# Performance work log

Measured on AMD Instinct MI355X. Metric: run time of the kernel, lower is better.

The kernel has to match this reference:

```python
import jax, jax.numpy as jnp
import numpy as np

B, M, N, L = 8, 384, 1536, 20  # batch, checks (detectors), error mechanisms, BP layers
ROW_W = 8  # check-node degree of sparse parity-check matrix H


def setup_inputs() -> dict:
    key = jax.random.key(0)
    ks = jax.random.split(key, 10)
    # Sparse binary check matrix: each row has exactly ROW_W ones (LDPC-like DEM).
    rng = np.random.default_rng(0)
    H_np = np.zeros((M, N), np.float32)
    for i in range(M):
        H_np[i, rng.choice(N, ROW_W, replace=False)] = 1.0
    H = jnp.asarray(H_np)
    llrs = jax.random.uniform(ks[0], (N,), minval=0.5, maxval=2.0)
    syndromes = jax.random.randint(ks[1], (B, M, 1), 0, 2).astype(jnp.float32)
    errors = jax.random.randint(ks[2], (B, N), 0, 2).astype(jnp.float32)
    # Per-layer learned weights (damped so 20 BP iterations stay numerically stable).
    weights_de = jax.random.uniform(ks[3], (L, M, N), minval=0.1, maxval=0.25)
    weights_llr = jax.random.uniform(ks[4], (L, N), minval=0.5, maxval=1.0)
    marg_weights_de = jax.random.uniform(ks[5], (M, N), minval=0.5, maxval=1.0)
    marg_weights_llr = jax.random.uniform(ks[6], (N,), minval=0.5, maxval=1.0)
    residual_weights = jax.random.uniform(ks[7], (L,), minval=0.0, maxval=0.1)
    rhos = jnp.ones((L,), jnp.float32) / L  # init: ones normalized by layers
    return dict(syndromes=syndromes, errors=errors, H=H, llrs=llrs,
                weights_de=weights_de, weights_llr=weights_llr,
                marg_weights_de=marg_weights_de, marg_weights_llr=marg_weights_llr,
                residual_weights=residual_weights, rhos=rhos)


def reference(syndromes, errors, H, llrs, weights_de, weights_llr,
              marg_weights_de, marg_weights_llr, residual_weights, rhos):
    sign = (1.0 - 2.0 * syndromes) * H          # (B,M,N): (-1)^syndrome masked by H
    one_minus_e = 1.0 - errors                  # (B,N)

    def step(msg_dn, per_layer):
        w_de, w_llr, res_w, rho = per_layer
        # --- error (variable) node update ---
        base = H * (llrs * w_llr)                                     # (M,N)
        msg_en = (base + jnp.sum(msg_dn * w_de, axis=1, keepdims=True)) * H - msg_dn
        # --- detector (check) node update: tanh-product with self-exclusion by division ---
        d = jnp.tanh(msg_en * 0.5)
        d = jnp.where(d == 0.0, 1.0, d)
        p = jnp.prod(d, axis=2, keepdims=True)                        # (B,M,1)
        msg_dn_new = 2.0 * jnp.arctanh(p / d) * sign + res_w * msg_dn
        # --- marginals (beliefs) + per-layer loss ---
        beliefs = jnp.sum(msg_dn_new * marg_weights_de, axis=1) + llrs * marg_weights_llr  # (B,N)
        loss_b = jnp.sum(jax.nn.softplus(beliefs) - one_minus_e * beliefs, axis=1) * rho   # (B,)
        return msg_dn_new, loss_b

    msg0 = jnp.zeros((syndromes.shape[0], H.shape[0], H.shape[1]), jnp.float32)
    _, losses = jax.lax.scan(step, msg0, (weights_de, weights_llr, residual_weights, rhos))
    return jnp.sum(losses) / syndromes.shape[0]  # scalar mean-over-batch loss
```

## Files before the change

### kernel.cpp

```cpp
#include <hip/hip_runtime.h>
#include <math.h>

#define MB 8
#define MM 384
#define NN 1536
#define LL 20
#define RW 8
#define HE 4
#define NE (MM*RW)
#define NT 768
#define VP 12
#define VG 3

#define SOFT_BAR() asm volatile("s_waitcnt lgkmcnt(0)\n\ts_barrier" ::: "memory")

static __device__ __forceinline__ float dpp_xor1(float x) {
    return __int_as_float(
        __builtin_amdgcn_mov_dpp(__float_as_int(x), 0xB1, 0xF, 0xF, true));
}

__global__ __launch_bounds__(256) void setup_kernel(
    const float* __restrict__ H,
    const float* __restrict__ llrs,
    const float* __restrict__ w_llr,
    const float* __restrict__ w_de,
    const float* __restrict__ marg_de,
    int*   __restrict__ col_pack,
    float* __restrict__ base_e,
    float* __restrict__ wde_vT,
    float* __restrict__ marg_vT,
    int*   __restrict__ gcnt,
    float* __restrict__ out) {
    const int m = blockIdx.x;
    const int t = threadIdx.x;
    const int w = t >> 6, lane = t & 63;
    __shared__ int s_qcol[4][RW];
    __shared__ int s_qcnt[4];
    __shared__ int s_col[RW];
    __shared__ int s_pos[RW];

    const float* row = H + (size_t)m * NN;
    int count = 0;
    for (int c0 = w * 384; c0 < (w + 1) * 384; c0 += 64) {
        float v = row[c0 + lane];
        unsigned long long mask = __ballot(v != 0.0f);
        if (v != 0.0f) {
            int pos = count + (int)__popcll(mask & ((1ull << lane) - 1ull));
            if (pos < RW) s_qcol[w][pos] = c0 + lane;
        }
        count += (int)__popcll(mask);
    }
    if (lane == 0) s_qcnt[w] = (count < RW) ? count : RW;
    __syncthreads();
    if (t == 0) {
        int off = 0;
        for (int q = 0; q < 4; ++q)
            for (int i = 0; i < s_qcnt[q]; ++i) {
                if (off < RW) s_col[off] = s_qcol[q][i];
                ++off;
            }
    }
    __syncthreads();

    if (t < RW) {
        int c = s_col[t];
        int pos = atomicAdd(&gcnt[c], 1);
        if (pos >= VP) pos = VP - 1;
        s_pos[t] = pos;
        col_pack[m * RW + t] = c | (pos << 16);
        marg_vT[((pos >> 2) * NN + c) * 4 + (pos & 3)] = marg_de[m * NN + c];
    }
    if (m == 0 && t == 0) out[0] = 0.0f;
    __syncthreads();

    for (int idx = t; idx < LL * RW; idx += 256) {
        int l = idx >> 3;
        int k = idx & 7;
        int c = s_col[k];
        int pos = s_pos[k];
        wde_vT[((l * VG + (pos >> 2)) * NN + c) * 4 + (pos & 3)] =
            w_de[(size_t)l * MM * NN + (size_t)m * NN + c];
        base_e[l * NE + m * RW + k] = llrs[c] * w_llr[l * NN + c];
    }
}

#define LAYER_BODY(lv, WC0, WC1, BC, WN0, WN1, BN)                            \
{                                                                             \
               \
    {                                                                         \
        int lb = ((lv) + 1 < LL) ? ((lv) + 1) : (LL - 1);                     \
        _Pragma("unroll")                                                     \
        for (int jg = 0; jg < VG; ++jg) {                                     \
            float4 a = ((const float4*)wde_vT)[(lb * VG + jg) * NN + t];      \
            WN0[jg*4+0]=a.x; WN0[jg*4+1]=a.y; WN0[jg*4+2]=a.z; WN0[jg*4+3]=a.w; \
            float4 c4 = ((const float4*)wde_vT)[(lb * VG + jg) * NN + t + NT];\
            WN1[jg*4+0]=c4.x; WN1[jg*4+1]=c4.y; WN1[jg*4+2]=c4.z; WN1[jg*4+3]=c4.w; \
        }                                                                     \
        const float4 bp4 = ((const float4*)(base_e_g + lb * NE))[t];          \
        BN[0]=bp4.x; BN[1]=bp4.y; BN[2]=bp4.z; BN[3]=bp4.w;                   \
    }                                                                         \
            \
    {                                                                         \
        float S0, S1, bel0 = bias[0], bel1 = bias[1];                         \
        {          \
            float4 a = ((const float4*)s_cN)[t];                              \
            S0    = a.x*WC0[0] + a.y*WC0[1] + a.z*WC0[2] + a.w*WC0[3];        \
            bel0 += a.x*mg0[0] + a.y*mg0[1] + a.z*mg0[2] + a.w*mg0[3];        \
            float4 c4 = ((const float4*)s_cN)[t + NT];                        \
            S1    = c4.x*WC1[0] + c4.y*WC1[1] + c4.z*WC1[2] + c4.w*WC1[3];    \
            bel1 += c4.x*mg1[0] + c4.y*mg1[1] + c4.z*mg1[2] + c4.w*mg1[3];    \
        }                                                                     \
        if (deg0 > 4) {                                                       \
            float4 a = ((const float4*)s_cN)[NN + t];                         \
            S0   += a.x*WC0[4] + a.y*WC0[5] + a.z*WC0[6] + a.w*WC0[7];        \
            bel0 += a.x*mg0[4] + a.y*mg0[5] + a.z*mg0[6] + a.w*mg0[7];        \
        }                                                                     \
        if (deg1 > 4) {                                                       \
            float4 c4 = ((const float4*)s_cN)[NN + t + NT];                   \
            S1   += c4.x*WC1[4] + c4.y*WC1[5] + c4.z*WC1[6] + c4.w*WC1[7];    \
            bel1 += c4.x*mg1[4] + c4.y*mg1[5] + c4.z*mg1[6] + c4.w*mg1[7];    \
        }                                                                     \
        if (deg0 > 8) {                                                       \
            float4 a = ((const float4*)s_cN)[2 * NN + t];                     \
            S0   += a.x*WC0[8] + a.y*WC0[9] + a.z*WC0[10] + a.w*WC0[11];      \
            bel0 += a.x*mg0[8] + a.y*mg0[9] + a.z*mg0[10] + a.w*mg0[11];      \
        }                                                                     \
        if (deg1 > 8) {                                                       \
            float4 c4 = ((const float4*)s_cN)[2 * NN + t + NT];               \
            S1   += c4.x*WC1[8] + c4.y*WC1[9] + c4.z*WC1[10] + c4.w*WC1[11];  \
            bel1 += c4.x*mg1[8] + c4.y*mg1[9] + c4.z*mg1[10] + c4.w*mg1[11];  \
        }                                                                     \
        s_S[t]      = S0;                                                     \
        s_S[t + NT] = S1;                                                     \
        if ((lv) > 0) {                                                       \
            const float rr = s_rho[(lv) - 1];                                 \
            float sp0 = fmaxf(bel0, 0.0f) + __logf(1.0f + __expf(-fabsf(bel0))); \
            float sp1 = fmaxf(bel1, 0.0f) + __logf(1.0f + __expf(-fabsf(bel1))); \
            loss += rr * ((sp0 - omeg[0] * bel0) + (sp1 - omeg[1] * bel1));   \
        }                                                                     \
    }                                                                         \
    SOFT_BAR();                \
    {                                                                         \
        const float rw_ = s_rw[(lv)];                                         \
        float d[HE];                                                          \
        _Pragma("unroll")                                                     \
        for (int k = 0; k < HE; ++k) {                                        \
            float te = BC[k] + s_S[col[k]] - msg[k];                          \
            float e  = __expf(te);                                            \
            float dd = 1.0f - 2.0f * __builtin_amdgcn_rcpf(e + 1.0f);         \
            dd = fminf(fmaxf(dd, -1.0f), 1.0f);                               \
            if (dd == 0.0f) dd = 1.0f;                                        \
            d[k] = dd;                                                        \
        }                                                                     \
        float pre2 = d[0] * d[1];                                             \
        float suf1 = d[2] * d[3];                                             \
        float p4   = pre2 * suf1;                                             \
        float pot  = dpp_xor1(p4);                                            \
        float ex[HE];                                                         \
        ex[0] = d[1] * suf1;                                                  \
        ex[1] = d[0] * suf1;                                                  \
        ex[2] = pre2 * d[3];                                                  \
        ex[3] = pre2 * d[2];                                                  \
        _Pragma("unroll")                                                     \
        for (int k = 0; k < HE; ++k) {                                        \
            float x  = ex[k] * pot;                                           \
            float r  = (1.0f + x) * __builtin_amdgcn_rcpf(1.0f - x);          \
            float nm = sgn * __logf(r) + rw_ * msg[k];                        \
            msg[k] = nm;                                                      \
            s_cN[esl[k]] = nm;                                                \
        }                                                                     \
    }                                                                         \
    SOFT_BAR();                  \
}

__global__ __launch_bounds__(NT) void bp_kernel(
    const float* __restrict__ synd,
    const float* __restrict__ errors,
    const float* __restrict__ llrs,
    const float* __restrict__ marg_llr,
    const float* __restrict__ res_w,
    const float* __restrict__ rhos,
    const int*   __restrict__ col_pack,
    const float* __restrict__ base_e_g,
    const float* __restrict__ wde_vT,
    const float* __restrict__ marg_vT,
    const int*   __restrict__ gdeg,
    float* __restrict__ out) {

    __shared__ float s_cN[NN * VP];
    __shared__ float s_S[NN];
    __shared__ float s_rw[LL];
    __shared__ float s_rho[LL];
    __shared__ float s_red[12];

    const int b = blockIdx.x;
    const int t = threadIdx.x;
    const int m = t >> 1;

    int col[HE], esl[HE];
    {
        const int4 cp = ((const int4*)col_pack)[t];
        int v[HE] = {cp.x, cp.y, cp.z, cp.w};
        #pragma unroll
        for (int k = 0; k < HE; ++k) {
            int c = v[k] & 0xFFFF, pos = v[k] >> 16;
            col[k] = c;
            esl[k] = ((pos >> 2) * NN + c) * 4 + (pos & 3);
        }
    }
    float msg[HE] = {0.0f, 0.0f, 0.0f, 0.0f};
    const float sgn = 1.0f - 2.0f * synd[b * MM + m];

    const int deg0 = gdeg[t];
    const int deg1 = gdeg[t + NT];
    float bias[2], omeg[2];
    #pragma unroll
    for (int i = 0; i < 2; ++i) {
        int n = t + i * NT;
        bias[i] = llrs[n] * marg_llr[n];
        omeg[i] = 1.0f - errors[b * NN + n];
    }

    float mg0[VP], mg1[VP];
    #pragma unroll
    for (int jg = 0; jg < VG; ++jg) {
        float4 a = ((const float4*)marg_vT)[jg * NN + t];
        mg0[jg*4+0] = a.x; mg0[jg*4+1] = a.y; mg0[jg*4+2] = a.z; mg0[jg*4+3] = a.w;
        float4 c4 = ((const float4*)marg_vT)[jg * NN + t + NT];
        mg1[jg*4+0] = c4.x; mg1[jg*4+1] = c4.y; mg1[jg*4+2] = c4.z; mg1[jg*4+3] = c4.w;
    }
    float wcA0[VP], wcA1[VP], wcB0[VP], wcB1[VP];
    #pragma unroll
    for (int jg = 0; jg < VG; ++jg) {
        float4 a = ((const float4*)wde_vT)[jg * NN + t];
        wcA0[jg*4+0] = a.x; wcA0[jg*4+1] = a.y; wcA0[jg*4+2] = a.z; wcA0[jg*4+3] = a.w;
        float4 c4 = ((const float4*)wde_vT)[jg * NN + t + NT];
        wcA1[jg*4+0] = c4.x; wcA1[jg*4+1] = c4.y; wcA1[jg*4+2] = c4.z; wcA1[jg*4+3] = c4.w;
    }
    float bcA[HE], bcB[HE];
    {
        const float4 bp4 = ((const float4*)base_e_g)[t];
        bcA[0] = bp4.x; bcA[1] = bp4.y; bcA[2] = bp4.z; bcA[3] = bp4.w;
    }

    #pragma unroll
    for (int j = 0; j < 6; ++j)
        ((float4*)s_cN)[j * NT + t] = make_float4(0.f, 0.f, 0.f, 0.f);
    if (t < LL) { s_rw[t] = res_w[t]; s_rho[t] = rhos[t]; }

    float loss = 0.0f;
    __syncthreads();

    for (int l = 0; l < LL; l += 2) {
        LAYER_BODY(l,     wcA0, wcA1, bcA, wcB0, wcB1, bcB);
        LAYER_BODY(l + 1, wcB0, wcB1, bcB, wcA0, wcA1, bcA);
    }

    {
        const float rr = s_rho[LL - 1];
        float bel0 = bias[0], bel1 = bias[1];
        {
            float4 a = ((const float4*)s_cN)[t];
            bel0 += a.x*mg0[0] + a.y*mg0[1] + a.z*mg0[2] + a.w*mg0[3];
            float4 c4 = ((const float4*)s_cN)[t + NT];
            bel1 += c4.x*mg1[0] + c4.y*mg1[1] + c4.z*mg1[2] + c4.w*mg1[3];
        }
        if (deg0 > 4) {
            float4 a = ((const float4*)s_cN)[NN + t];
            bel0 += a.x*mg0[4] + a.y*mg0[5] + a.z*mg0[6] + a.w*mg0[7];
        }
        if (deg1 > 4) {
            float4 c4 = ((const float4*)s_cN)[NN + t + NT];
            bel1 += c4.x*mg1[4] + c4.y*mg1[5] + c4.z*mg1[6] + c4.w*mg1[7];
        }
        if (deg0 > 8) {
            float4 a = ((const float4*)s_cN)[2 * NN + t];
            bel0 += a.x*mg0[8] + a.y*mg0[9] + a.z*mg0[10] + a.w*mg0[11];
        }
        if (deg1 > 8) {
            float4 c4 = ((const float4*)s_cN)[2 * NN + t + NT];
            bel1 += c4.x*mg1[8] + c4.y*mg1[9] + c4.z*mg1[10] + c4.w*mg1[11];
        }
        float sp0 = fmaxf(bel0, 0.0f) + __logf(1.0f + __expf(-fabsf(bel0)));
        float sp1 = fmaxf(bel1, 0.0f) + __logf(1.0f + __expf(-fabsf(bel1)));
        loss += rr * ((sp0 - omeg[0] * bel0) + (sp1 - omeg[1] * bel1));
    }

    #pragma unroll
    for (int off = 32; off > 0; off >>= 1)
        loss += __shfl_down(loss, off, 64);
    int wave = t >> 6, lane = t & 63;
    if (lane == 0) s_red[wave] = loss;
    __syncthreads();
    if (t == 0) {
        float tot = 0.0f;
        #pragma unroll
        for (int w = 0; w < 12; ++w) tot += s_red[w];
        atomicAdd(out, tot * (1.0f / (float)MB));
    }
}

extern "C" void kernel_launch(void* const* d_in, const int* in_sizes, int n_in,
                              void* d_out, int out_size, void* d_ws, size_t ws_size,
                              hipStream_t stream) {
    const float* synd     = (const float*)d_in[0];
    const float* errors   = (const float*)d_in[1];
    const float* H        = (const float*)d_in[2];
    const float* llrs     = (const float*)d_in[3];
    const float* w_de     = (const float*)d_in[4];
    const float* w_llr    = (const float*)d_in[5];
    const float* marg_de  = (const float*)d_in[6];
    const float* marg_llr = (const float*)d_in[7];
    const float* res_w    = (const float*)d_in[8];
    const float* rhos     = (const float*)d_in[9];
    float* out = (float*)d_out;

    float* wde_vT  = (float*)d_ws;
    float* marg_vT = wde_vT + (size_t)LL * VG * NN * 4;
    int*   gcnt    = (int*)(marg_vT + VG * NN * 4);
    float* base_e  = (float*)(gcnt + NN);
    int*   col_pack= (int*)(base_e + (size_t)LL * NE);

    hipMemsetAsync(gcnt, 0, NN * sizeof(int), stream);
    setup_kernel<<<MM, 256, 0, stream>>>(H, llrs, w_llr, w_de, marg_de,
                                         col_pack, base_e, wde_vT, marg_vT,
                                         gcnt, out);
    bp_kernel<<<MB, NT, 0, stream>>>(synd, errors, llrs, marg_llr, res_w, rhos,
                                     col_pack, base_e, wde_vT, marg_vT, gcnt, out);
}
```

Baseline: 145.5 us.

## Carry BP messages in log2 units, hoist LDS reads, move weight prefetch past barrier

Messages are carried in log2 units. Base LLR terms are pre-scaled by log2(e) and the marginal weights by ln2 in setup, so the check-node update can use native exp2/log2 instructions without extra multiplies. The reciprocal-then-log step becomes a difference of two hardware log2 calls. The next layer's weight and base prefetch now sits after the first barrier, next to hoisted s_S gathers, to overlap global loads with the check update. Residual and rho scalars are read from global memory instead of LDS, and the shared arrays holding them are removed. The two-log form adds a transcendental per edge, and moving the prefetch raises register pressure.

```diff
diff --git a/kernel.cpp b/kernel.cpp
--- a/kernel.cpp
+++ b/kernel.cpp
@@ -11,6 +11,9 @@
 #define NT 768
 #define VP 12
 #define VG 3
+
+#define LOG2E 1.44269504f
+#define LN2   0.69314718f
 
 #define SOFT_BAR() asm volatile("s_waitcnt lgkmcnt(0)\n\ts_barrier" ::: "memory")
 
@@ -68,7 +71,7 @@
         if (pos >= VP) pos = VP - 1;
         s_pos[t] = pos;
         col_pack[m * RW + t] = c | (pos << 16);
-        marg_vT[((pos >> 2) * NN + c) * 4 + (pos & 3)] = marg_de[m * NN + c];
+        marg_vT[((pos >> 2) * NN + c) * 4 + (pos & 3)] = marg_de[m * NN + c] * LN2;
     }
     if (m == 0 && t == 0) out[0] = 0.0f;
     __syncthreads();
@@ -80,28 +83,15 @@
         int pos = s_pos[k];
         wde_vT[((l * VG + (pos >> 2)) * NN + c) * 4 + (pos & 3)] =
             w_de[(size_t)l * MM * NN + (size_t)m * NN + c];
-        base_e[l * NE + m * RW + k] = llrs[c] * w_llr[l * NN + c];
+        base_e[l * NE + m * RW + k] = llrs[c] * w_llr[l * NN + c] * LOG2E;
     }
 }
 
 #define LAYER_BODY(lv, WC0, WC1, BC, WN0, WN1, BN)                            \
 {                                                                             \
-               \
-    {                                                                         \
-        int lb = ((lv) + 1 < LL) ? ((lv) + 1) : (LL - 1);                     \
-        _Pragma("unroll")                                                     \
-        for (int jg = 0; jg < VG; ++jg) {                                     \
-            float4 a = ((const float4*)wde_vT)[(lb * VG + jg) * NN + t];      \
-            WN0[jg*4+0]=a.x; WN0[jg*4+1]=a.y; WN0[jg*4+2]=a.z; WN0[jg*4+3]=a.w; \
-            float4 c4 = ((const float4*)wde_vT)[(lb * VG + jg) * NN + t + NT];\
-            WN1[jg*4+0]=c4.x; WN1[jg*4+1]=c4.y; WN1[jg*4+2]=c4.z; WN1[jg*4+3]=c4.w; \
-        }                                                                     \
-        const float4 bp4 = ((const float4*)(base_e_g + lb * NE))[t];          \
-        BN[0]=bp4.x; BN[1]=bp4.y; BN[2]=bp4.z; BN[3]=bp4.w;                   \
-    }                                                                         \
-            \
-    {                                                                         \
-        float S0, S1, bel0 = bias[0], bel1 = bias[1];                         \
+    float bel0 = bias[0], bel1 = bias[1];                                     \
+    {             \
+        float S0, S1;                                                         \
         {          \
             float4 a = ((const float4*)s_cN)[t];                              \
             S0    = a.x*WC0[0] + a.y*WC0[1] + a.z*WC0[2] + a.w*WC0[3];        \
@@ -132,21 +122,39 @@
         }                                                                     \
         s_S[t]      = S0;                                                     \
         s_S[t + NT] = S1;                                                     \
+    }                                                                         \
+    SOFT_BAR();                \
+    {                                                                         \
+                                     \
+        float ss[HE];                                                         \
+        _Pragma("unroll")                                                     \
+        for (int k = 0; k < HE; ++k) ss[k] = s_S[col[k]];                     \
+                        \
         if ((lv) > 0) {                                                       \
-            const float rr = s_rho[(lv) - 1];                                 \
+            const float rr = rhos[(lv) - 1];                                  \
             float sp0 = fmaxf(bel0, 0.0f) + __logf(1.0f + __expf(-fabsf(bel0))); \
             float sp1 = fmaxf(bel1, 0.0f) + __logf(1.0f + __expf(-fabsf(bel1))); \
             loss += rr * ((sp0 - omeg[0] * bel0) + (sp1 - omeg[1] * bel1));   \
         }                                                                     \
-    }                                                                         \
-    SOFT_BAR();                \
-    {                                                                         \
-        const float rw_ = s_rw[(lv)];                                         \
+               \
+        {                                                                     \
+            int lb = ((lv) + 1 < LL) ? ((lv) + 1) : (LL - 1);                 \
+            _Pragma("unroll")                                                 \
+            for (int jg = 0; jg < VG; ++jg) {                                 \
+                float4 a = ((const float4*)wde_vT)[(lb * VG + jg) * NN + t];  \
+                WN0[jg*4+0]=a.x; WN0[jg*4+1]=a.y; WN0[jg*4+2]=a.z; WN0[jg*4+3]=a.w; \
+                float4 c4 = ((const float4*)wde_vT)[(lb * VG + jg) * NN + t + NT]; \
+                WN1[jg*4+0]=c4.x; WN1[jg*4+1]=c4.y; WN1[jg*4+2]=c4.z; WN1[jg*4+3]=c4.w; \
+            }                                                                 \
+            const float4 bp4 = ((const float4*)(base_e_g + lb * NE))[t];      \
+            BN[0]=bp4.x; BN[1]=bp4.y; BN[2]=bp4.z; BN[3]=bp4.w;               \
+        }                                                                     \
+        const float rw_ = res_w[(lv)];                                        \
         float d[HE];                                                          \
         _Pragma("unroll")                                                     \
         for (int k = 0; k < HE; ++k) {                                        \
-            float te = BC[k] + s_S[col[k]] - msg[k];                          \
-            float e  = __expf(te);                                            \
+            float te = BC[k] + ss[k] - msg[k];               \
+            float e  = __builtin_amdgcn_exp2f(te);                            \
             float dd = 1.0f - 2.0f * __builtin_amdgcn_rcpf(e + 1.0f);         \
             dd = fminf(fmaxf(dd, -1.0f), 1.0f);                               \
             if (dd == 0.0f) dd = 1.0f;                                        \
@@ -164,8 +172,9 @@
         _Pragma("unroll")                                                     \
         for (int k = 0; k < HE; ++k) {                                        \
             float x  = ex[k] * pot;                                           \
-            float r  = (1.0f + x) * __builtin_amdgcn_rcpf(1.0f - x);          \
-            float nm = sgn * __logf(r) + rw_ * msg[k];                        \
+            float la = __builtin_amdgcn_logf(1.0f + x);                       \
+            float lb2 = __builtin_amdgcn_logf(1.0f - x);                      \
+            float nm = sgn * (la - lb2) + rw_ * msg[k];      \
             msg[k] = nm;                                                      \
             s_cN[esl[k]] = nm;                                                \
         }                                                                     \
@@ -189,8 +198,6 @@
 
     __shared__ float s_cN[NN * VP];
     __shared__ float s_S[NN];
-    __shared__ float s_rw[LL];
-    __shared__ float s_rho[LL];
     __shared__ float s_red[12];
 
     const int b = blockIdx.x;
@@ -246,7 +253,6 @@
     #pragma unroll
     for (int j = 0; j < 6; ++j)
         ((float4*)s_cN)[j * NT + t] = make_float4(0.f, 0.f, 0.f, 0.f);
-    if (t < LL) { s_rw[t] = res_w[t]; s_rho[t] = rhos[t]; }
 
     float loss = 0.0f;
     __syncthreads();
@@ -257,7 +263,7 @@
     }
 
     {
-        const float rr = s_rho[LL - 1];
+        const float rr = rhos[LL - 1];
         float bel0 = bias[0], bel1 = bias[1];
         {
             float4 a = ((const float4*)s_cN)[t];
```

New measurement: 141.2 us. 3.0% less time.
